# Kernel tuning notes

Hardware: AMD Instinct MI355X
Metric: run time of the kernel (lower is better)

The kernel has to match this reference:

```python
import jax, jax.numpy as jnp
import numpy as np

N, E = 40000, 640000
EMB, HID, H, TXT = 128, 128, 4, 384
C = HID // H  # per-head channels = 32


def _prelu(x, a):
    return jnp.where(x >= 0, x, a * x)


def _layernorm(x, g, b, eps=1e-5):
    m = jnp.mean(x, axis=-1, keepdims=True)
    v = jnp.mean((x - m) ** 2, axis=-1, keepdims=True)
    return (x - m) / jnp.sqrt(v + eps) * g + b


def _gat_conv(h, src, dst, W, att_src, att_dst, bias):
    # PyG GATConv (concat=True, eval mode): lin has no bias, self-loops already in src/dst.
    xh = (h @ W.T).reshape(N, H, C)                      # [N,H,C]
    a_src = jnp.sum(xh * att_src, axis=-1)               # [N,H]
    a_dst = jnp.sum(xh * att_dst, axis=-1)               # [N,H]
    alpha = jax.nn.leaky_relu(a_src[src] + a_dst[dst], negative_slope=0.2)  # [Et,H]
    amax = jax.ops.segment_max(alpha, dst, num_segments=N)
    ex = jnp.exp(alpha - amax[dst])
    denom = jax.ops.segment_sum(ex, dst, num_segments=N)
    coef = ex / denom[dst]                               # scatter-softmax over dst
    out = jax.ops.segment_sum(xh[src] * coef[:, :, None], dst, num_segments=N)
    return out.reshape(N, H * C) + bias


def setup_inputs() -> dict:
    key = jax.random.key(0)
    ks = jax.random.split(key, 20)
    nrm = lambda k, s, sc=0.05: jax.random.normal(k, s, jnp.float32) * sc
    inp = {
        "x": nrm(ks[0], (N, EMB), 1.0),
        "num_x": nrm(ks[1], (N, 1), 1.0),
        "num_mask": jnp.ones((N,), jnp.float32),
        "txt_x": nrm(ks[2], (N, TXT), 1.0),
        "txt_mask": jnp.ones((N,), jnp.float32),
        "edge_index": jax.random.randint(ks[3], (2, E), 0, N, jnp.int32),
        "num_proj_w": nrm(ks[4], (EMB, 1)), "num_proj_b": jnp.zeros((EMB,), jnp.float32),
        "txt_proj_w": nrm(ks[5], (EMB, TXT)), "txt_proj_b": jnp.zeros((EMB,), jnp.float32),
        "node_proj_w": nrm(ks[6], (HID, EMB)), "node_proj_b": jnp.zeros((HID,), jnp.float32),
        "prelu0_a": jnp.full((HID,), 0.25, jnp.float32),
        "conv1_w": nrm(ks[7], (HID, HID)), "att_src1": nrm(ks[8], (H, C)), "att_dst1": nrm(ks[9], (H, C)), "bias1": jnp.zeros((HID,), jnp.float32),
        "norm1_g": jnp.ones((HID,), jnp.float32), "norm1_b": jnp.zeros((HID,), jnp.float32),
        "prelu1_a": jnp.full((HID,), 0.25, jnp.float32),
        "conv2_w": nrm(ks[10], (HID, HID)), "att_src2": nrm(ks[11], (H, C)), "att_dst2": nrm(ks[12], (H, C)), "bias2": jnp.zeros((HID,), jnp.float32),
        "norm2_g": jnp.ones((HID,), jnp.float32), "norm2_b": jnp.zeros((HID,), jnp.float32),
        "prelu2_a": jnp.full((HID,), 0.25, jnp.float32),
        "out_w": nrm(ks[13], (1, HID)), "out_b": jnp.zeros((1,), jnp.float32),
    }
    return inp


def reference(x, num_x, num_mask, txt_x, txt_mask, edge_index,
              num_proj_w, num_proj_b, txt_proj_w, txt_proj_b,
              node_proj_w, node_proj_b, prelu0_a,
              conv1_w, att_src1, att_dst1, bias1, norm1_g, norm1_b, prelu1_a,
              conv2_w, att_src2, att_dst2, bias2, norm2_g, norm2_b, prelu2_a,
              out_w, out_b):
    # add self loops (PyG GATConv default)
    loop = jnp.arange(N, dtype=edge_index.dtype)
    src = jnp.concatenate([edge_index[0], loop])
    dst = jnp.concatenate([edge_index[1], loop])

    h = (num_x * num_mask[:, None]) @ num_proj_w.T + num_proj_b
    h = h + (txt_x * txt_mask[:, None]) @ txt_proj_w.T + txt_proj_b
    h = h + x @ node_proj_w.T + node_proj_b
    h = _prelu(h, prelu0_a)

    h = _gat_conv(h, src, dst, conv1_w, att_src1, att_dst1, bias1)
    h = _prelu(_layernorm(h, norm1_g, norm1_b), prelu1_a)  # dropout: eval mode -> identity

    h = _gat_conv(h, src, dst, conv2_w, att_src2, att_dst2, bias2)
    h = _prelu(_layernorm(h, norm2_g, norm2_b), prelu2_a)

    return (h @ out_w.T + out_b).squeeze(-1)  # [N]
```

## Files before the change

### kernel.cpp

```cpp
#include <hip/hip_runtime.h>
#include <stdint.h>

typedef unsigned short u16;
typedef unsigned int u32;
typedef __attribute__((ext_vector_type(8))) short bf16x8;
typedef __attribute__((ext_vector_type(4))) float f32x4;

__device__ __forceinline__ float bf2f(u32 u) {
    union { u32 i; float f; } v; v.i = u << 16; return v.f;
}
__device__ __forceinline__ u16 f2bf(float f) {
    u32 x = __float_as_uint(f);
    return (u16)((x + 0x7fffu + ((x >> 16) & 1u)) >> 16);
}
__device__ __forceinline__ float wred_sum(float v) {
#pragma unroll
    for (int o = 32; o > 0; o >>= 1) v += __shfl_xor(v, o, 64);
    return v;
}
__device__ __forceinline__ bf16x8 cvt8(float4 a, float4 b) {
    union { uint4 u; bf16x8 v; } t;
    t.u.x = (u32)f2bf(a.x) | ((u32)f2bf(a.y) << 16);
    t.u.y = (u32)f2bf(a.z) | ((u32)f2bf(a.w) << 16);
    t.u.z = (u32)f2bf(b.x) | ((u32)f2bf(b.y) << 16);
    t.u.w = (u32)f2bf(b.z) | ((u32)f2bf(b.w) << 16);
    return t.v;
}
__device__ __forceinline__ bf16x8 ld16B(const u16* p, size_t off) {
    union { uint4 u; bf16x8 b; } t; t.u = *(const uint4*)(p + off); return t.b;
}
__device__ __forceinline__ void glds16(const void* g, void* l) {
    __builtin_amdgcn_global_load_lds(
        (const __attribute__((address_space(1))) void*)g,
        (__attribute__((address_space(3))) void*)l, 16, 0, 0);
}
__device__ __forceinline__ void stageW_glds(const u16* __restrict__ W, int ldk, int koff,
                                            u16* swl, int tid) {
    int w64 = tid >> 6;
#pragma unroll
    for (int it = 0; it < 8; ++it) {
        int row = it * 16 + (tid >> 4);
        int sphys = tid & 15;
        int ssrc = sphys ^ (row & 7);
        const u16* g = W + (size_t)row * ldk + koff + ssrc * 8;
        u16* dst = swl + (size_t)(it * 256 + w64 * 64) * 8;
        glds16(g, dst);
    }
}
__device__ __forceinline__ bf16x8 ldBx(const u16* swl, int ct, int ks, int l16, int quad) {
    int row = ct * 16 + l16;
    int slot = (ks * 4 + quad) ^ (row & 7);
    union { uint4 u; bf16x8 b; } t;
    t.u = *(const uint4*)&swl[row * 128 + slot * 8];
    return t.b;
}
__device__ __forceinline__ void stageA_glds(const float* __restrict__ Ab, int ldk, int koff,
                                            float* sAw, int lane) {
#pragma unroll
    for (int it = 0; it < 8; ++it) {
        int rl = it * 2 + (lane >> 5);
        int sl = (lane & 31) ^ (rl & 7);
        const float* g = Ab + (size_t)rl * ldk + koff + sl * 4;
        glds16(g, sAw + it * 256);
    }
}

__global__ void k_cvtw(const float* __restrict__ s0, const float* __restrict__ s1,
                       const float* __restrict__ s2, const float* __restrict__ s3,
                       u16* __restrict__ d, int n0, int n1, int n2, int n3,
                       int* __restrict__ deg, int N) {
    int tix = blockIdx.x * 256 + threadIdx.x;
    if (tix < N) deg[tix] = 0;
    int i = tix * 8;
    int t = i;
    const float* s;
    if (t < n0) s = s0 + t;
    else if ((t -= n0) < n1) s = s1 + t;
    else if ((t -= n1) < n2) s = s2 + t;
    else if ((t -= n2) < n3) s = s3 + t;
    else return;
    float4 a = *(const float4*)s, b = *(const float4*)(s + 4);
    uint4 v;
    v.x = (u32)f2bf(a.x) | ((u32)f2bf(a.y) << 16);
    v.y = (u32)f2bf(a.z) | ((u32)f2bf(a.w) << 16);
    v.z = (u32)f2bf(b.x) | ((u32)f2bf(b.y) << 16);
    v.w = (u32)f2bf(b.z) | ((u32)f2bf(b.w) << 16);
    *(uint4*)(d + i) = v;
}

__global__ void k_hist(const int* __restrict__ dst, int E, int* __restrict__ deg) {
    int e = blockIdx.x * 256 + threadIdx.x;
    if (e < E) atomicAdd(&deg[dst[e]], 1);
}
__global__ __launch_bounds__(1024) void k_scanA(const int* __restrict__ deg, int n,
                                                int* __restrict__ out, int* __restrict__ bsum) {
    __shared__ int wsum[16];
    int t = threadIdx.x, w = t >> 6, lane = t & 63;
    int i0 = blockIdx.x * 4096 + t * 4;
    int4 v = make_int4(0, 0, 0, 0);
    if (i0 + 3 < n) v = *(const int4*)&deg[i0];
    else {
        if (i0 < n)     v.x = deg[i0];
        if (i0 + 1 < n) v.y = deg[i0 + 1];
        if (i0 + 2 < n) v.z = deg[i0 + 2];
    }
    int tsum = v.x + v.y + v.z + v.w;
    int s = tsum;
#pragma unroll
    for (int o = 1; o < 64; o <<= 1) { int u = __shfl_up(s, o, 64); if (lane >= o) s += u; }
    if (lane == 63) wsum[w] = s;
    __syncthreads();
    if (w == 0 && lane < 16) {
        int ws = wsum[lane];
#pragma unroll
        for (int o = 1; o < 16; o <<= 1) { int u = __shfl_up(ws, o, 64); if (lane >= o) ws += u; }
        wsum[lane] = ws;
    }
    __syncthreads();
    int woff = (w == 0) ? 0 : wsum[w - 1];
    int p = woff + s - tsum;
    if (i0 + 3 < n) {
        int4 o4; o4.x = p; o4.y = p + v.x; o4.z = p + v.x + v.y; o4.w = p + v.x + v.y + v.z;
        *(int4*)&out[i0] = o4;
    } else {
        int pp = p;
        if (i0 < n)     { out[i0] = pp;     pp += v.x; }
        if (i0 + 1 < n) { out[i0 + 1] = pp; pp += v.y; }
        if (i0 + 2 < n) { out[i0 + 2] = pp; }
    }
    if (t == 0) bsum[blockIdx.x] = wsum[15];
}
__global__ void k_scanB(int* __restrict__ bsum, int nb, int* __restrict__ total) {
    int lane = threadIdx.x;
    int v = (lane < nb) ? bsum[lane] : 0;
    int s = v;
#pragma unroll
    for (int o = 1; o < 64; o <<= 1) { int u = __shfl_up(s, o, 64); if (lane >= o) s += u; }
    if (lane < nb) bsum[lane] = s - v;
    if (lane == 63) total[0] = s;
}
__global__ void k_scanC(int* __restrict__ rowptr, int* __restrict__ cursor,
                        const int* __restrict__ boff, int n) {
    int i = blockIdx.x * 256 + threadIdx.x;
    if (i < n) {
        int r = rowptr[i] + boff[i >> 12];
        rowptr[i] = r; cursor[i] = r;
    }
}
__global__ void k_scatter(const int* __restrict__ srcp, const int* __restrict__ dstp, int E,
                          int* __restrict__ cursor, int* __restrict__ col) {
    int e = blockIdx.x * 256 + threadIdx.x;
    if (e < E) {
        int p = atomicAdd(&cursor[dstp[e]], 1);
        col[p] = srcp[e];
    }
}

__global__ __launch_bounds__(256) void k_fused1(
    const float* __restrict__ x, const float* __restrict__ numx, const float* __restrict__ numm,
    const float* __restrict__ txt, const float* __restrict__ txtm,
    const float* __restrict__ numw, const float* __restrict__ numb,
    const float* __restrict__ txtb, const float* __restrict__ nodeb,
    const float* __restrict__ pa,
    const u16* __restrict__ txtwb, const u16* __restrict__ nodewb, const u16* __restrict__ w1b,
    const float* __restrict__ atts, const float* __restrict__ attd,
    u16* __restrict__ xh, float* __restrict__ asrc, float* __restrict__ adst) {
    __shared__ u16 swl[128 * 128];
    __shared__ float sA[4][2048];
    int tid = threadIdx.x, w = tid >> 6, lane = tid & 63, quad = lane >> 4, l16 = lane & 15;
    int nb = blockIdx.x * 64 + w * 16;

    float* sAw = &sA[w][0];
    u16* shw = (u16*)sAw;
    const float* tBase = txt + (size_t)nb * 384;
    const float* xBase = x + (size_t)nb * 128;

    f32x4 acc[8];
#pragma unroll
    for (int ct = 0; ct < 8; ++ct) { f32x4 z = {0.f, 0.f, 0.f, 0.f}; acc[ct] = z; }

#define CHUNK(Wp, ldk, koff, Ab)                                                \
    {                                                                           \
        stageW_glds(Wp, ldk, koff, swl, tid);                                   \
        stageA_glds(Ab, ldk, koff, sAw, lane);                                  \
        __syncthreads();                              \
        _Pragma("unroll")                                                       \
        for (int ks = 0; ks < 4; ++ks) {                                        \
            int s0 = (ks * 8 + quad * 2) ^ (l16 & 7);                           \
            int s1 = (ks * 8 + quad * 2 + 1) ^ (l16 & 7);                       \
            float4 fa = *(const float4*)&sAw[l16 * 128 + s0 * 4];               \
            float4 fb = *(const float4*)&sAw[l16 * 128 + s1 * 4];               \
            bf16x8 a0 = cvt8(fa, fb);                                           \
            _Pragma("unroll")                                                   \
            for (int ct = 0; ct < 8; ++ct)                                      \
                acc[ct] = __builtin_amdgcn_mfma_f32_16x16x32_bf16(              \
                    a0, ldBx(swl, ct, ks, l16, quad), acc[ct], 0, 0, 0);        \
        }                                                                       \
        __syncthreads();                        \
    }

    CHUNK(txtwb, 384, 0,   tBase)
    CHUNK(txtwb, 384, 128, tBase)
    CHUNK(txtwb, 384, 256, tBase)
#pragma unroll
    for (int r = 0; r < 4; ++r) {
        float tm = txtm[nb + quad * 4 + r];
#pragma unroll
        for (int ct = 0; ct < 8; ++ct) acc[ct][r] *= tm;
    }
    CHUNK(nodewb, 128, 0, xBase)
#undef CHUNK

    float nm[4];
#pragma unroll
    for (int r = 0; r < 4; ++r) {
        int n = nb + quad * 4 + r;
        nm[r] = numx[n] * numm[n];
    }
#pragma unroll
    for (int ct = 0; ct < 8; ++ct) {
        int c = ct * 16 + l16;
        float cw = numw[c];
        float cb = numb[c] + txtb[c] + nodeb[c];
        float pav = pa[c];
#pragma unroll
        for (int r = 0; r < 4; ++r) {
            float v = acc[ct][r] + nm[r] * cw + cb;
            v = v >= 0.f ? v : pav * v;
            int rr = quad * 4 + r;
            int ps = (c >> 3) ^ (rr & 7);
            shw[rr * 128 + ps * 8 + (c & 7)] = f2bf(v);
        }
    }
    __syncthreads();
    stageW_glds(w1b, 128, 0, swl, tid);
    __syncthreads();
    f32x4 a2[8];
#pragma unroll
    for (int ct = 0; ct < 8; ++ct) { f32x4 z = {0.f, 0.f, 0.f, 0.f}; a2[ct] = z; }
#pragma unroll
    for (int ks = 0; ks < 4; ++ks) {
        bf16x8 a0 = ld16B(shw, l16 * 128 + (((ks * 4 + quad) ^ (l16 & 7)) << 3));
#pragma unroll
        for (int ct = 0; ct < 8; ++ct)
            a2[ct] = __builtin_amdgcn_mfma_f32_16x16x32_bf16(
                a0, ldBx(swl, ct, ks, l16, quad), a2[ct], 0, 0, 0);
    }
#pragma unroll
    for (int ct = 0; ct < 8; ++ct) {
        int c = ct * 16 + l16;
#pragma unroll
        for (int r = 0; r < 4; ++r)
            xh[(size_t)(nb + quad * 4 + r) * 128 + c] = f2bf(a2[ct][r]);
    }
    float as_[8], ad_[8];
#pragma unroll
    for (int ct = 0; ct < 8; ++ct) {
        int c = ct * 16 + l16;
        as_[ct] = atts[c];
        ad_[ct] = attd[c];
    }
#pragma unroll
    for (int hh = 0; hh < 4; ++hh) {
        float vs[4], vd[4];
#pragma unroll
        for (int r = 0; r < 4; ++r) {
            vs[r] = a2[2 * hh][r] * as_[2 * hh] + a2[2 * hh + 1][r] * as_[2 * hh + 1];
            vd[r] = a2[2 * hh][r] * ad_[2 * hh] + a2[2 * hh + 1][r] * ad_[2 * hh + 1];
        }
#pragma unroll
        for (int o = 1; o <= 8; o <<= 1) {
#pragma unroll
            for (int r = 0; r < 4; ++r) {
                vs[r] += __shfl_xor(vs[r], o, 64);
                vd[r] += __shfl_xor(vd[r], o, 64);
            }
        }
        if ((l16 >> 2) == hh) {
            int r = l16 & 3;
            float ss = (r == 0) ? vs[0] : (r == 1) ? vs[1] : (r == 2) ? vs[2] : vs[3];
            float dd = (r == 0) ? vd[0] : (r == 1) ? vd[1] : (r == 2) ? vd[2] : vd[3];
            int n = nb + quad * 4 + r;
            asrc[n * 4 + hh] = ss;
            adst[n * 4 + hh] = dd;
        }
    }
}

__global__ __launch_bounds__(256) void k_xh(
    const u16* __restrict__ h, const u16* __restrict__ Wb,
    const float* __restrict__ att_s, const float* __restrict__ att_d,
    u16* __restrict__ xh, float* __restrict__ asrc, float* __restrict__ adst) {
    __shared__ u16 swl[128 * 128];
    int tid = threadIdx.x;
    int w = tid >> 6, lane = tid & 63, quad = lane >> 4, l16 = lane & 15;
    int nb = blockIdx.x * 64 + w * 16;

    stageW_glds(Wb, 128, 0, swl, tid);
    const u16* hrow = h + (size_t)(nb + l16) * 128 + quad * 8;
    uint4 A0 = *(const uint4*)(hrow);
    uint4 A1 = *(const uint4*)(hrow + 32);
    uint4 A2 = *(const uint4*)(hrow + 64);
    uint4 A3 = *(const uint4*)(hrow + 96);
    f32x4 acc[8];
#pragma unroll
    for (int ct = 0; ct < 8; ++ct) { f32x4 z = {0.f, 0.f, 0.f, 0.f}; acc[ct] = z; }
    __syncthreads();
    union { uint4 u; bf16x8 b; } t0, t1, t2, t3;
    t0.u = A0; t1.u = A1; t2.u = A2; t3.u = A3;
#pragma unroll
    for (int ct = 0; ct < 8; ++ct)
        acc[ct] = __builtin_amdgcn_mfma_f32_16x16x32_bf16(
            t0.b, ldBx(swl, ct, 0, l16, quad), acc[ct], 0, 0, 0);
#pragma unroll
    for (int ct = 0; ct < 8; ++ct)
        acc[ct] = __builtin_amdgcn_mfma_f32_16x16x32_bf16(
            t1.b, ldBx(swl, ct, 1, l16, quad), acc[ct], 0, 0, 0);
#pragma unroll
    for (int ct = 0; ct < 8; ++ct)
        acc[ct] = __builtin_amdgcn_mfma_f32_16x16x32_bf16(
            t2.b, ldBx(swl, ct, 2, l16, quad), acc[ct], 0, 0, 0);
#pragma unroll
    for (int ct = 0; ct < 8; ++ct)
        acc[ct] = __builtin_amdgcn_mfma_f32_16x16x32_bf16(
            t3.b, ldBx(swl, ct, 3, l16, quad), acc[ct], 0, 0, 0);
#pragma unroll
    for (int ct = 0; ct < 8; ++ct) {
        int c = ct * 16 + l16;
#pragma unroll
        for (int r = 0; r < 4; ++r) {
            int n = nb + quad * 4 + r;
            xh[(size_t)n * 128 + c] = f2bf(acc[ct][r]);
        }
    }
    float as_[8], ad_[8];
#pragma unroll
    for (int ct = 0; ct < 8; ++ct) {
        int c = ct * 16 + l16;
        as_[ct] = att_s[c];
        ad_[ct] = att_d[c];
    }
#pragma unroll
    for (int hh = 0; hh < 4; ++hh) {
        float vs[4], vd[4];
#pragma unroll
        for (int r = 0; r < 4; ++r) {
            vs[r] = acc[2 * hh][r] * as_[2 * hh] + acc[2 * hh + 1][r] * as_[2 * hh + 1];
            vd[r] = acc[2 * hh][r] * ad_[2 * hh] + acc[2 * hh + 1][r] * ad_[2 * hh + 1];
        }
#pragma unroll
        for (int o = 1; o <= 8; o <<= 1) {
#pragma unroll
            for (int r = 0; r < 4; ++r) {
                vs[r] += __shfl_xor(vs[r], o, 64);
                vd[r] += __shfl_xor(vd[r], o, 64);
            }
        }
        if ((l16 >> 2) == hh) {
            int r = l16 & 3;
            float ss = (r == 0) ? vs[0] : (r == 1) ? vs[1] : (r == 2) ? vs[2] : vs[3];
            float dd = (r == 0) ? vd[0] : (r == 1) ? vd[1] : (r == 2) ? vd[2] : vd[3];
            int n = nb + quad * 4 + r;
            asrc[n * 4 + hh] = ss;
            adst[n * 4 + hh] = dd;
        }
    }
}

__global__ __launch_bounds__(64) void k_agg(
    const u16* __restrict__ xh, const float* __restrict__ asrc, const float* __restrict__ adst,
    const int* __restrict__ rowptr, const int* __restrict__ col,
    const float* __restrict__ bias, const float* __restrict__ g, const float* __restrict__ b,
    const float* __restrict__ pa, u16* __restrict__ hnext,
    const float* __restrict__ outw, const float* __restrict__ outb, float* __restrict__ outy,
    int is_final) {
    __shared__ int   scol[64];
    __shared__ float scoef[64][4];
    int n = blockIdx.x, lane = threadIdx.x;
    int beg = rowptr[n], end = rowptr[n + 1];
    const float4* asrc4 = (const float4*)asrc;

    float4 adv = ((const float4*)adst)[n];
    float ad[4] = { adv.x, adv.y, adv.z, adv.w };
    float4 asv = asrc4[n];
    float els[4];
#pragma unroll
    for (int h = 0; h < 4; h++) {
        float a = ((const float*)&asv)[h] + ad[h];
        a = a >= 0.f ? a : 0.2f * a;
        els[h] = __expf(a);
    }
    int hh = lane >> 4;
    u32 vself = ((const u32*)(xh + (size_t)n * 128))[lane];
    float ac0[8], ac1[8];
#pragma unroll
    for (int q = 0; q < 8; ++q) { ac0[q] = 0.f; ac1[q] = 0.f; }
    ac0[0] = els[hh] * bf2f(vself & 0xffffu);
    ac1[0] = els[hh] * bf2f(vself >> 16);
    float l[4] = { 0.f, 0.f, 0.f, 0.f };

    for (int base = beg; base < end; base += 64) {
        int e = base + lane;
        int cnt = min(64, end - base);
        if (e < end) {
            int s = col[e];
            float4 av = asrc4[s];
            scol[lane] = s;
            float cf[4];
#pragma unroll
            for (int h = 0; h < 4; h++) {
                float a = ((const float*)&av)[h] + ad[h];
                a = a >= 0.f ? a : 0.2f * a;
                cf[h] = __expf(a);
                l[h] += cf[h];
            }
            *(float4*)scoef[lane] = make_float4(cf[0], cf[1], cf[2], cf[3]);
        }
        __syncthreads();
        int j = 0;
        for (; j + 7 < cnt; j += 8) {
            int ss[8]; float cc[8]; u32 vv[8];
#pragma unroll
            for (int q = 0; q < 8; ++q) { ss[q] = scol[j + q]; cc[q] = scoef[j + q][hh]; }
#pragma unroll
            for (int q = 0; q < 8; ++q) vv[q] = ((const u32*)(xh + (size_t)ss[q] * 128))[lane];
#pragma unroll
            for (int q = 0; q < 8; ++q) {
                ac0[q] += cc[q] * bf2f(vv[q] & 0xffffu);
                ac1[q] += cc[q] * bf2f(vv[q] >> 16);
            }
        }
        for (; j + 3 < cnt; j += 4) {
            int ss[4]; float cc[4]; u32 vv[4];
#pragma unroll
            for (int q = 0; q < 4; ++q) { ss[q] = scol[j + q]; cc[q] = scoef[j + q][hh]; }
#pragma unroll
            for (int q = 0; q < 4; ++q) vv[q] = ((const u32*)(xh + (size_t)ss[q] * 128))[lane];
#pragma unroll
            for (int q = 0; q < 4; ++q) {
                ac0[q] += cc[q] * bf2f(vv[q] & 0xffffu);
                ac1[q] += cc[q] * bf2f(vv[q] >> 16);
            }
        }
        for (; j < cnt; ++j) {
            int s0 = scol[j];
            float c0 = scoef[j][hh];
            u32 v0 = ((const u32*)(xh + (size_t)s0 * 128))[lane];
            ac0[0] += c0 * bf2f(v0 & 0xffffu);
            ac1[0] += c0 * bf2f(v0 >> 16);
        }
        __syncthreads();
    }
    float acc0 = 0.f, acc1 = 0.f;
#pragma unroll
    for (int q = 0; q < 8; ++q) { acc0 += ac0[q]; acc1 += ac1[q]; }

    float L[4];
#pragma unroll
    for (int h = 0; h < 4; h++) L[h] = wred_sum(l[h]) + els[h];
    float inv = 1.f / L[hh];
    acc0 *= inv;
    acc1 *= inv;

    int c0i = 2 * lane;
    float2 bi = *(const float2*)(bias + c0i);
    acc0 += bi.x; acc1 += bi.y;

    float mean = wred_sum(acc0 + acc1) * (1.f / 128.f);
    float d0 = acc0 - mean, d1 = acc1 - mean;
    float var = wred_sum(d0 * d0 + d1 * d1) * (1.f / 128.f);
    float rstd = rsqrtf(var + 1e-5f);
    float2 gg = *(const float2*)(g + c0i);
    float2 bb = *(const float2*)(b + c0i);
    float2 pp = *(const float2*)(pa + c0i);
    float y0 = d0 * rstd * gg.x + bb.x;
    float y1 = d1 * rstd * gg.y + bb.y;
    y0 = y0 >= 0.f ? y0 : pp.x * y0;
    y1 = y1 >= 0.f ? y1 : pp.y * y1;

    if (is_final) {
        float2 ow = *(const float2*)(outw + c0i);
        float dot = wred_sum(y0 * ow.x + y1 * ow.y);
        if (lane == 0) outy[n] = dot + outb[0];
    } else {
        ((u32*)(hnext + (size_t)n * 128))[lane] = (u32)f2bf(y0) | ((u32)f2bf(y1) << 16);
    }
}

extern "C" void kernel_launch(void* const* d_in, const int* in_sizes, int n_in,
                              void* d_out, int out_size, void* d_ws, size_t ws_size,
                              hipStream_t stream) {
    const int N = in_sizes[2];
    const int E = in_sizes[5] / 2;

    const float* x      = (const float*)d_in[0];
    const float* numx   = (const float*)d_in[1];
    const float* numm   = (const float*)d_in[2];
    const float* txt    = (const float*)d_in[3];
    const float* txtm   = (const float*)d_in[4];
    const int*   ei     = (const int*)d_in[5];
    const float* numw   = (const float*)d_in[6];
    const float* numb   = (const float*)d_in[7];
    const float* txtw   = (const float*)d_in[8];
    const float* txtb   = (const float*)d_in[9];
    const float* nodew  = (const float*)d_in[10];
    const float* nodeb  = (const float*)d_in[11];
    const float* pa0    = (const float*)d_in[12];
    const float* conv1w = (const float*)d_in[13];
    const float* atts1  = (const float*)d_in[14];
    const float* attd1  = (const float*)d_in[15];
    const float* bias1  = (const float*)d_in[16];
    const float* g1     = (const float*)d_in[17];
    const float* b1     = (const float*)d_in[18];
    const float* pa1    = (const float*)d_in[19];
    const float* conv2w = (const float*)d_in[20];
    const float* atts2  = (const float*)d_in[21];
    const float* attd2  = (const float*)d_in[22];
    const float* bias2  = (const float*)d_in[23];
    const float* g2     = (const float*)d_in[24];
    const float* b2     = (const float*)d_in[25];
    const float* pa2    = (const float*)d_in[26];
    const float* outw   = (const float*)d_in[27];
    const float* outb   = (const float*)d_in[28];

    const int* srcp = ei;
    const int* dstp = ei + E;

    const int szTxtw = in_sizes[8];
    const int szNode = in_sizes[10];
    const int szW1   = in_sizes[13];
    const int szW2   = in_sizes[20];
    const int szWAll = szTxtw + szNode + szW1 + szW2;

    char* p = (char*)d_ws;
    auto alloc = [&](size_t bytes) -> void* {
        void* q = (void*)p;
        p += (bytes + 255) & ~(size_t)255;
        return q;
    };
    u16*   hA     = (u16*)alloc((size_t)N * 128 * 2);
    u16*   hB     = (u16*)alloc((size_t)N * 128 * 2);
    float* asrc   = (float*)alloc((size_t)N * 4 * 4);
    float* adst   = (float*)alloc((size_t)N * 4 * 4);
    int*   deg    = (int*)alloc((size_t)N * 4);
    int*   rowptr = (int*)alloc((size_t)(N + 1) * 4);
    int*   cursor = (int*)alloc((size_t)N * 4);
    int*   col    = (int*)alloc((size_t)E * 4);
    int*   bsum   = (int*)alloc(64 * 4);
    u16*   wbf    = (u16*)alloc((size_t)szWAll * 2);

    u16* txtwb  = wbf;
    u16* nodewb = wbf + szTxtw;
    u16* w1b    = nodewb + szNode;
    u16* w2b    = w1b + szW1;

    const int gCvt = ((szWAll / 8 > N ? szWAll / 8 : N) + 255) / 256;
    k_cvtw<<<gCvt, 256, 0, stream>>>(
        txtw, nodew, conv1w, conv2w, wbf, szTxtw, szNode, szW1, szW2, deg, N);

    const int nbScan = (N + 4095) / 4096;
    k_hist<<<(E + 255) / 256, 256, 0, stream>>>(dstp, E, deg);
    k_scanA<<<nbScan, 1024, 0, stream>>>(deg, N, rowptr, bsum);
    k_scanB<<<1, 64, 0, stream>>>(bsum, nbScan, rowptr + N);
    k_scanC<<<(N + 255) / 256, 256, 0, stream>>>(rowptr, cursor, bsum, N);
    k_scatter<<<(E + 255) / 256, 256, 0, stream>>>(srcp, dstp, E, cursor, col);

    const int gProj = N / 64;

    k_fused1<<<gProj, 256, 0, stream>>>(x, numx, numm, txt, txtm, numw, numb,
                                        txtb, nodeb, pa0,
                                        txtwb, nodewb, w1b, atts1, attd1, hB, asrc, adst);
    k_agg<<<N, 64, 0, stream>>>(hB, asrc, adst, rowptr, col, bias1, g1, b1, pa1,
                                hA, nullptr, nullptr, nullptr, 0);

    k_xh<<<gProj, 256, 0, stream>>>(hA, w2b, atts2, attd2, hB, asrc, adst);
    k_agg<<<N, 64, 0, stream>>>(hB, asrc, adst, rowptr, col, bias2, g2, b2, pa2,
                                nullptr, outw, outb, (float*)d_out, 1);
}
```

Baseline: 316.2 us.

## Fuse layer-2 linear projection and attention logits into first aggregation kernel

```diff
diff --git a/kernel.cpp b/kernel.cpp
--- a/kernel.cpp
+++ b/kernel.cpp
@@ -287,95 +287,18 @@
     }
 }
 
-__global__ __launch_bounds__(256) void k_xh(
-    const u16* __restrict__ h, const u16* __restrict__ Wb,
-    const float* __restrict__ att_s, const float* __restrict__ att_d,
-    u16* __restrict__ xh, float* __restrict__ asrc, float* __restrict__ adst) {
-    __shared__ u16 swl[128 * 128];
-    int tid = threadIdx.x;
-    int w = tid >> 6, lane = tid & 63, quad = lane >> 4, l16 = lane & 15;
-    int nb = blockIdx.x * 64 + w * 16;
-
-    stageW_glds(Wb, 128, 0, swl, tid);
-    const u16* hrow = h + (size_t)(nb + l16) * 128 + quad * 8;
-    uint4 A0 = *(const uint4*)(hrow);
-    uint4 A1 = *(const uint4*)(hrow + 32);
-    uint4 A2 = *(const uint4*)(hrow + 64);
-    uint4 A3 = *(const uint4*)(hrow + 96);
-    f32x4 acc[8];
-#pragma unroll
-    for (int ct = 0; ct < 8; ++ct) { f32x4 z = {0.f, 0.f, 0.f, 0.f}; acc[ct] = z; }
-    __syncthreads();
-    union { uint4 u; bf16x8 b; } t0, t1, t2, t3;
-    t0.u = A0; t1.u = A1; t2.u = A2; t3.u = A3;
-#pragma unroll
-    for (int ct = 0; ct < 8; ++ct)
-        acc[ct] = __builtin_amdgcn_mfma_f32_16x16x32_bf16(
-            t0.b, ldBx(swl, ct, 0, l16, quad), acc[ct], 0, 0, 0);
-#pragma unroll
-    for (int ct = 0; ct < 8; ++ct)
-        acc[ct] = __builtin_amdgcn_mfma_f32_16x16x32_bf16(
-            t1.b, ldBx(swl, ct, 1, l16, quad), acc[ct], 0, 0, 0);
-#pragma unroll
-    for (int ct = 0; ct < 8; ++ct)
-        acc[ct] = __builtin_amdgcn_mfma_f32_16x16x32_bf16(
-            t2.b, ldBx(swl, ct, 2, l16, quad), acc[ct], 0, 0, 0);
-#pragma unroll
-    for (int ct = 0; ct < 8; ++ct)
-        acc[ct] = __builtin_amdgcn_mfma_f32_16x16x32_bf16(
-            t3.b, ldBx(swl, ct, 3, l16, quad), acc[ct], 0, 0, 0);
-#pragma unroll
-    for (int ct = 0; ct < 8; ++ct) {
-        int c = ct * 16 + l16;
-#pragma unroll
-        for (int r = 0; r < 4; ++r) {
-            int n = nb + quad * 4 + r;
-            xh[(size_t)n * 128 + c] = f2bf(acc[ct][r]);
-        }
-    }
-    float as_[8], ad_[8];
-#pragma unroll
-    for (int ct = 0; ct < 8; ++ct) {
-        int c = ct * 16 + l16;
-        as_[ct] = att_s[c];
-        ad_[ct] = att_d[c];
-    }
-#pragma unroll
-    for (int hh = 0; hh < 4; ++hh) {
-        float vs[4], vd[4];
-#pragma unroll
-        for (int r = 0; r < 4; ++r) {
-            vs[r] = acc[2 * hh][r] * as_[2 * hh] + acc[2 * hh + 1][r] * as_[2 * hh + 1];
-            vd[r] = acc[2 * hh][r] * ad_[2 * hh] + acc[2 * hh + 1][r] * ad_[2 * hh + 1];
-        }
-#pragma unroll
-        for (int o = 1; o <= 8; o <<= 1) {
-#pragma unroll
-            for (int r = 0; r < 4; ++r) {
-                vs[r] += __shfl_xor(vs[r], o, 64);
-                vd[r] += __shfl_xor(vd[r], o, 64);
-            }
-        }
-        if ((l16 >> 2) == hh) {
-            int r = l16 & 3;
-            float ss = (r == 0) ? vs[0] : (r == 1) ? vs[1] : (r == 2) ? vs[2] : vs[3];
-            float dd = (r == 0) ? vd[0] : (r == 1) ? vd[1] : (r == 2) ? vd[2] : vd[3];
-            int n = nb + quad * 4 + r;
-            asrc[n * 4 + hh] = ss;
-            adst[n * 4 + hh] = dd;
-        }
-    }
-}
-
 __global__ __launch_bounds__(64) void k_agg(
     const u16* __restrict__ xh, const float* __restrict__ asrc, const float* __restrict__ adst,
     const int* __restrict__ rowptr, const int* __restrict__ col,
     const float* __restrict__ bias, const float* __restrict__ g, const float* __restrict__ b,
-    const float* __restrict__ pa, u16* __restrict__ hnext,
+    const float* __restrict__ pa,
+    const u16* __restrict__ w2b, const float* __restrict__ atts2, const float* __restrict__ attd2,
+    u16* __restrict__ xh2, float* __restrict__ asrc2, float* __restrict__ adst2,
     const float* __restrict__ outw, const float* __restrict__ outb, float* __restrict__ outy,
     int is_final) {
     __shared__ int   scol[64];
     __shared__ float scoef[64][4];
+    __shared__ float srow[128];
     int n = blockIdx.x, lane = threadIdx.x;
     int beg = rowptr[n], end = rowptr[n + 1];
     const float4* asrc4 = (const float4*)asrc;
@@ -483,7 +406,40 @@
         float dot = wred_sum(y0 * ow.x + y1 * ow.y);
         if (lane == 0) outy[n] = dot + outb[0];
     } else {
-        ((u32*)(hnext + (size_t)n * 128))[lane] = (u32)f2bf(y0) | ((u32)f2bf(y1) << 16);
+        srow[c0i]     = bf2f((u32)f2bf(y0));
+        srow[c0i + 1] = bf2f((u32)f2bf(y1));
+        __syncthreads();
+        const u16* w2r = w2b + (size_t)c0i * 128;
+        float dd0 = 0.f, dd1 = 0.f;
+#pragma unroll
+        for (int kb = 0; kb < 16; ++kb) {
+            bf16x8 wa = ld16B(w2r, kb * 8);
+            bf16x8 wb = ld16B(w2r, 128 + kb * 8);
+            float4 ha = *(const float4*)&srow[kb * 8];
+            float4 hb = *(const float4*)&srow[kb * 8 + 4];
+            dd0 += ha.x * bf2f((u16)wa[0]) + ha.y * bf2f((u16)wa[1])
+                 + ha.z * bf2f((u16)wa[2]) + ha.w * bf2f((u16)wa[3])
+                 + hb.x * bf2f((u16)wa[4]) + hb.y * bf2f((u16)wa[5])
+                 + hb.z * bf2f((u16)wa[6]) + hb.w * bf2f((u16)wa[7]);
+            dd1 += ha.x * bf2f((u16)wb[0]) + ha.y * bf2f((u16)wb[1])
+                 + ha.z * bf2f((u16)wb[2]) + ha.w * bf2f((u16)wb[3])
+                 + hb.x * bf2f((u16)wb[4]) + hb.y * bf2f((u16)wb[5])
+                 + hb.z * bf2f((u16)wb[6]) + hb.w * bf2f((u16)wb[7]);
+        }
+        ((u32*)(xh2 + (size_t)n * 128))[lane] = (u32)f2bf(dd0) | ((u32)f2bf(dd1) << 16);
+        float2 a2s = *(const float2*)(atts2 + c0i);
+        float2 a2d = *(const float2*)(attd2 + c0i);
+        float vs = dd0 * a2s.x + dd1 * a2s.y;
+        float vd = dd0 * a2d.x + dd1 * a2d.y;
+#pragma unroll
+        for (int o = 1; o <= 8; o <<= 1) {
+            vs += __shfl_xor(vs, o, 64);
+            vd += __shfl_xor(vd, o, 64);
+        }
+        if ((lane & 15) == 0) {
+            asrc2[n * 4 + hh] = vs;
+            adst2[n * 4 + hh] = vd;
+        }
     }
 }
 
@@ -542,6 +498,8 @@
     u16*   hB     = (u16*)alloc((size_t)N * 128 * 2);
     float* asrc   = (float*)alloc((size_t)N * 4 * 4);
     float* adst   = (float*)alloc((size_t)N * 4 * 4);
+    float* asrc2  = (float*)alloc((size_t)N * 4 * 4);
+    float* adst2  = (float*)alloc((size_t)N * 4 * 4);
     int*   deg    = (int*)alloc((size_t)N * 4);
     int*   rowptr = (int*)alloc((size_t)(N + 1) * 4);
     int*   cursor = (int*)alloc((size_t)N * 4);
@@ -571,9 +529,10 @@
                                         txtb, nodeb, pa0,
                                         txtwb, nodewb, w1b, atts1, attd1, hB, asrc, adst);
     k_agg<<<N, 64, 0, stream>>>(hB, asrc, adst, rowptr, col, bias1, g1, b1, pa1,
-                                hA, nullptr, nullptr, nullptr, 0);
-
-    k_xh<<<gProj, 256, 0, stream>>>(hA, w2b, atts2, attd2, hB, asrc, adst);
-    k_agg<<<N, 64, 0, stream>>>(hB, asrc, adst, rowptr, col, bias2, g2, b2, pa2,
-                                nullptr, outw, outb, (float*)d_out, 1);
-}
+                                w2b, atts2, attd2, hA, asrc2, adst2,
+                                nullptr, nullptr, nullptr, 0);
+
+    k_agg<<<N, 64, 0, stream>>>(hA, asrc2, adst2, rowptr, col, bias2, g2, b2, pa2,
+                                nullptr, nullptr, nullptr, nullptr, nullptr, nullptr,
+                                outw, outb, (float*)d_out, 1);
+}
```

After: 470.0 us. 1.49x slower.
